# Performance work log

Hardware: AMD Instinct MI355X
Metric: run time of the kernel (lower is better)

## Reference

```python
import jax, jax.numpy as jnp
import numpy as np

B, T, HID = 2, 2048, 2048
H, HKV, HD = 16, 4, 128
GROUPS = H // HKV  # num_query_groups
THETA = 10000.0
SCALE = HD ** -0.5


def setup_inputs() -> dict:
    key = jax.random.key(0)
    ks = jax.random.split(key, 5)
    std = 0.02
    return {
        "x": jax.random.normal(ks[0], (B, T, HID), jnp.float32),
        "Wq": jax.random.normal(ks[1], (HID, H * HD), jnp.float32) * std,
        "Wk": jax.random.normal(ks[2], (HID, HKV * HD), jnp.float32) * std,
        "Wv": jax.random.normal(ks[3], (HID, HKV * HD), jnp.float32) * std,
        "Wo": jax.random.normal(ks[4], (H * HD, HID), jnp.float32) * std,
    }


def _rope(x):
    # x: [B, heads, T, HD]; standard LLaMA-style rotate-half RoPE
    t = x.shape[2]
    inv_freq = 1.0 / (THETA ** (jnp.arange(0, HD, 2, dtype=jnp.float32) / HD))  # [HD/2]
    ang = jnp.arange(t, dtype=jnp.float32)[:, None] * inv_freq[None, :]  # [T, HD/2]
    cos = jnp.concatenate([jnp.cos(ang), jnp.cos(ang)], axis=-1)[None, None]  # [1,1,T,HD]
    sin = jnp.concatenate([jnp.sin(ang), jnp.sin(ang)], axis=-1)[None, None]
    x1, x2 = jnp.split(x, 2, axis=-1)
    rot = jnp.concatenate([-x2, x1], axis=-1)
    return x * cos + rot * sin


def reference(x, Wq, Wk, Wv, Wo):
    b, t, _ = x.shape
    q = (x @ Wq).reshape(b, t, H, HD).transpose(0, 2, 1, 3)      # [B,H,T,HD]
    k = (x @ Wk).reshape(b, t, HKV, HD).transpose(0, 2, 1, 3)    # [B,HKV,T,HD]
    v = (x @ Wv).reshape(b, t, HKV, HD).transpose(0, 2, 1, 3)
    q = _rope(q)
    k = _rope(k)
    # GQA: repeat_interleave kv heads along head dim
    k = jnp.repeat(k, GROUPS, axis=1)  # [B,H,T,HD]
    v = jnp.repeat(v, GROUPS, axis=1)
    scores = jnp.einsum("bhqd,bhkd->bhqk", q, k) * SCALE  # [B,H,T,T]
    causal = jnp.tril(jnp.ones((t, t), dtype=bool))
    scores = jnp.where(causal[None, None], scores, jnp.finfo(scores.dtype).min)
    attn = jax.nn.softmax(scores, axis=-1)
    out = jnp.einsum("bhqk,bhkd->bhqd", attn, v)  # [B,H,T,HD]
    out = out.transpose(0, 2, 1, 3).reshape(b, t, H * HD)
    return out @ Wo
```

## Files before the change

kernel.cpp:

```cpp
#include <hip/hip_runtime.h>
#include <hip/hip_bf16.h>

#define B_   2
#define T_   2048
#define HID_ 2048
#define H_   16
#define HKV_ 4
#define HD_  128
#define NQKV 3072
#define M_   4096
#define SCALE_ 0.08838834764831845f

using f32x4 = __attribute__((ext_vector_type(4))) float;
using s16x8 = __attribute__((ext_vector_type(8))) short;

typedef const __attribute__((address_space(1))) unsigned int* gptr_t;
typedef __attribute__((address_space(3))) unsigned int* lptr_t;

__device__ __forceinline__ unsigned short f2bf(float f) {
  __hip_bfloat16 h = __float2bfloat16(f);
  return *reinterpret_cast<unsigned short*>(&h);
}
__device__ __forceinline__ float bf2f(unsigned short u) {
  union { unsigned int u; float f; } x;
  x.u = ((unsigned int)u) << 16;
  return x.f;
}

__global__ void cast_bf16_k(const float* __restrict__ in, unsigned short* __restrict__ out, int n4) {
  int i = blockIdx.x * 256 + threadIdx.x;
  if (i >= n4) return;
  float4 v = ((const float4*)in)[i];
  ushort4 o;
  o.x = f2bf(v.x); o.y = f2bf(v.y); o.z = f2bf(v.z); o.w = f2bf(v.w);
  ((ushort4*)out)[i] = o;
}

__global__ void transpose_cast_k(const float* __restrict__ in, unsigned short* __restrict__ out,
                                 int R, int C) {
  __shared__ float tile[32][33];
  const int tc = blockIdx.x * 32, tr = blockIdx.y * 32;
  const int lx = threadIdx.x & 31, ly = threadIdx.x >> 5;
#pragma unroll
  for (int i = 0; i < 32; i += 8) tile[ly + i][lx] = in[(long)(tr + ly + i) * C + tc + lx];
  __syncthreads();
#pragma unroll
  for (int i = 0; i < 32; i += 8)
    out[(long)(tc + ly + i) * R + tr + lx] = f2bf(tile[lx][ly + i]);
}

__global__ void transpose_v_k(const unsigned short* __restrict__ qkv, unsigned short* __restrict__ vtp) {
  __shared__ unsigned short tile[32][33];
  const int b = blockIdx.z;
  const int t0 = blockIdx.x * 32, n0 = blockIdx.y * 32;
  const int lx = threadIdx.x & 31, ly = threadIdx.x >> 5;
#pragma unroll
  for (int i = 0; i < 32; i += 8)
    tile[ly + i][lx] = qkv[(long)(b * T_ + t0 + ly + i) * NQKV + 2560 + n0 + lx];
  __syncthreads();
#pragma unroll
  for (int i = 0; i < 32; i += 8)
    vtp[(long)(b * 512 + n0 + ly + i) * T_ + t0 + lx] = tile[lx][ly + i];
}

__global__ void rope_table_k(float* __restrict__ cosT, float* __restrict__ sinT) {
  int idx = blockIdx.x * 256 + threadIdx.x;
  int tt = idx >> 6, i = idx & 63;
  float inv = powf(10000.0f, -(float)i * (1.0f / 64.0f));
  float ang = (float)tt * inv;
  cosT[idx] = cosf(ang);
  sinT[idx] = sinf(ang);
}

__global__ void rope_apply_k(unsigned short* __restrict__ qkv,
                             const float* __restrict__ cosT, const float* __restrict__ sinT) {
  int idx = blockIdx.x * 256 + threadIdx.x;
  int i = idx & 63;
  int r = idx >> 6;
  int hh = r % 20;
  int m = r / 20;
  int tt = m & (T_ - 1);
  int col = (hh < 16) ? hh * 128 + i : 2048 + (hh - 16) * 128 + i;
  float scl = (hh < 16) ? SCALE_ : 1.0f;
  unsigned short* p = qkv + (long)m * NQKV + col;
  float x0 = bf2f(p[0]), x1 = bf2f(p[64]);
  float c = cosT[tt * 64 + i], s = sinT[tt * 64 + i];
  p[0]  = f2bf((x0 * c - x1 * s) * scl);
  p[64] = f2bf((x1 * c + x0 * s) * scl);
}

template <bool BF16OUT>
__global__ __launch_bounds__(256) void gemm_bt(const short* __restrict__ A, const short* __restrict__ Bt,
                                               void* __restrict__ Cv, int M, int N, int K) {
  __shared__ short lA[4096];
  __shared__ short lB[4096];
  const int t = threadIdx.x;
  const int l = t & 63;
  const int w = t >> 6;
  const int wr = (w >> 1) * 64, wc = (w & 1) * 64;
  const int lr = l & 15, lk = (l >> 4) * 8;

  const short* Ag = A + (long)(blockIdx.x * 128 + (t >> 2)) * K + (t & 3) * 8;
  const short* Bg = Bt + (long)(blockIdx.y * 128 + (t >> 2)) * K + (t & 3) * 8;

  f32x4 acc[4][4] = {};

  for (int k0 = 0; k0 < K; k0 += 32) {
    __builtin_amdgcn_global_load_lds((gptr_t)(Ag + k0),                (lptr_t)&lA[t * 8],        16, 0, 0);
    __builtin_amdgcn_global_load_lds((gptr_t)(Ag + (long)64 * K + k0), (lptr_t)&lA[2048 + t * 8], 16, 0, 0);
    __builtin_amdgcn_global_load_lds((gptr_t)(Bg + k0),                (lptr_t)&lB[t * 8],        16, 0, 0);
    __builtin_amdgcn_global_load_lds((gptr_t)(Bg + (long)64 * K + k0), (lptr_t)&lB[2048 + t * 8], 16, 0, 0);
    __syncthreads();
    s16x8 af[4], bfr[4];
#pragma unroll
    for (int m = 0; m < 4; ++m) af[m] = *(const s16x8*)&lA[(wr + m * 16 + lr) * 32 + lk];
#pragma unroll
    for (int n = 0; n < 4; ++n) bfr[n] = *(const s16x8*)&lB[(wc + n * 16 + lr) * 32 + lk];
#pragma unroll
    for (int m = 0; m < 4; ++m)
#pragma unroll
      for (int n = 0; n < 4; ++n)
        acc[m][n] = __builtin_amdgcn_mfma_f32_16x16x32_bf16(af[m], bfr[n], acc[m][n], 0, 0, 0);
    __syncthreads();
  }

#pragma unroll
  for (int m = 0; m < 4; ++m) {
    const int row0 = blockIdx.x * 128 + wr + m * 16 + (l >> 4) * 4;
#pragma unroll
    for (int n = 0; n < 4; ++n) {
      const int col = blockIdx.y * 128 + wc + n * 16 + lr;
#pragma unroll
      for (int r = 0; r < 4; ++r) {
        float v = acc[m][n][r];
        if constexpr (BF16OUT)
          ((unsigned short*)Cv)[(long)(row0 + r) * N + col] = f2bf(v);
        else
          ((float*)Cv)[(long)(row0 + r) * N + col] = v;
      }
    }
  }
}

__global__ __launch_bounds__(256) void attn_kernel(const short* __restrict__ qkv,
                                                   const short* __restrict__ vt,
                                                   unsigned short* __restrict__ outp) {
  const int pj = blockIdx.x;
  const int bh = blockIdx.y;
  const int b = bh >> 4, h = bh & 15, hkv = h >> 2;
  const int tid = threadIdx.x, w = tid >> 6, l = tid & 63;
  const int lr = l & 15, lg = l >> 4;

  __shared__ short lK[2][8192];
  __shared__ short lP[4][16 * 72];

  const short* kb = qkv + (long)(b * T_) * NQKV + 2048 + hkv * HD_;
  const short* vb = vt + (long)(b * 512 + hkv * HD_) * T_;
  short* pw = &lP[w][0];

  auto STAGE = [&](int buf, int kvt) {
#pragma unroll
    for (int i = 0; i < 4; ++i) {
      int flat16 = i * 256 + tid;
      int r = flat16 >> 4;
      int cb = (flat16 & 15) << 4;
      int scb = cb ^ ((r & 7) << 4);
      const short* src = kb + (long)(kvt * 64 + r) * NQKV + (scb >> 1);
      __builtin_amdgcn_global_load_lds((gptr_t)src, (lptr_t)&lK[buf][flat16 * 8], 16, 0, 0);
    }
  };

#pragma unroll 1
  for (int ph = 0; ph < 2; ++ph) {
    const int qtile = ph ? 31 - pj : pj;
    const int ntiles = qtile + 1;

    const short* qp = qkv + (long)(b * T_ + qtile * 64 + w * 16 + lr) * NQKV + h * HD_;
    s16x8 qf[4];
#pragma unroll
    for (int ks = 0; ks < 4; ++ks) qf[ks] = *(const s16x8*)(qp + ks * 32 + lg * 8);

    f32x4 o[8] = {};
    float mrun[4], lrun[4];
#pragma unroll
    for (int r = 0; r < 4; ++r) { mrun[r] = -1e30f; lrun[r] = 0.f; }

    STAGE(0, 0);
    __syncthreads();
    int cur = 0;

    for (int kvt = 0; kvt < ntiles; ++kvt) {
      if (kvt + 1 < ntiles) STAGE(cur ^ 1, kvt + 1);

      const char* lkb = (const char*)&lK[cur][0];
      f32x4 s[4] = {};
#pragma unroll
      for (int nb = 0; nb < 4; ++nb) {
        const int row = nb * 16 + lr;
        const int rb = row * 256;
        const int xr = (row & 7) << 4;
#pragma unroll
        for (int ks = 0; ks < 4; ++ks) {
          s16x8 kf = *(const s16x8*)(lkb + (rb + ((ks * 64 + lg * 16) ^ xr)));
          s[nb] = __builtin_amdgcn_mfma_f32_16x16x32_bf16(qf[ks], kf, s[nb], 0, 0, 0);
        }
      }
      if (kvt == qtile) {
#pragma unroll
        for (int nb = 0; nb < 4; ++nb)
#pragma unroll
          for (int r = 0; r < 4; ++r)
            if (nb * 16 + lr > w * 16 + lg * 4 + r) s[nb][r] = -1e30f;
      }
      float sc[4];
#pragma unroll
      for (int r = 0; r < 4; ++r) {
        float v = fmaxf(fmaxf(s[0][r], s[1][r]), fmaxf(s[2][r], s[3][r]));
        v = fmaxf(v, __shfl_xor(v, 1));
        v = fmaxf(v, __shfl_xor(v, 2));
        v = fmaxf(v, __shfl_xor(v, 4));
        v = fmaxf(v, __shfl_xor(v, 8));
        float mnew = fmaxf(mrun[r], v);
        sc[r] = __expf(mrun[r] - mnew);
        mrun[r] = mnew;
      }
      float ps[4] = {0.f, 0.f, 0.f, 0.f};
#pragma unroll
      for (int nb = 0; nb < 4; ++nb)
#pragma unroll
        for (int r = 0; r < 4; ++r) {
          float p = __expf(s[nb][r] - mrun[r]);
          s[nb][r] = p;
          ps[r] += p;
        }
#pragma unroll
      for (int r = 0; r < 4; ++r) {
        ps[r] += __shfl_xor(ps[r], 1);
        ps[r] += __shfl_xor(ps[r], 2);
        ps[r] += __shfl_xor(ps[r], 4);
        ps[r] += __shfl_xor(ps[r], 8);
        lrun[r] = lrun[r] * sc[r] + ps[r];
      }
#pragma unroll
      for (int db = 0; db < 8; ++db)
#pragma unroll
        for (int r = 0; r < 4; ++r) o[db][r] *= sc[r];
#pragma unroll
      for (int nb = 0; nb < 4; ++nb)
#pragma unroll
        for (int r = 0; r < 4; ++r)
          pw[(lg * 4 + r) * 72 + nb * 16 + lr] = (short)f2bf(s[nb][r]);
#pragma unroll
      for (int ks2 = 0; ks2 < 2; ++ks2) {
        s16x8 pf = *(const s16x8*)&pw[lr * 72 + ks2 * 32 + lg * 8];
#pragma unroll
        for (int db = 0; db < 8; ++db) {
          s16x8 vf = *(const s16x8*)(vb + (long)(db * 16 + lr) * T_ + kvt * 64 + ks2 * 32 + lg * 8);
          o[db] = __builtin_amdgcn_mfma_f32_16x16x32_bf16(pf, vf, o[db], 0, 0, 0);
        }
      }
      __syncthreads();
      cur ^= 1;
    }

    unsigned short* ob = outp + (long)(b * T_ + qtile * 64 + w * 16) * HID_ + h * HD_;
#pragma unroll
    for (int db = 0; db < 8; ++db)
#pragma unroll
      for (int r = 0; r < 4; ++r)
        ob[(long)(lg * 4 + r) * HID_ + db * 16 + lr] = f2bf(o[db][r] / lrun[r]);
  }
}

extern "C" void kernel_launch(void* const* d_in, const int* in_sizes, int n_in,
                              void* d_out, int out_size, void* d_ws, size_t ws_size,
                              hipStream_t stream) {
  (void)in_sizes; (void)n_in; (void)out_size; (void)ws_size;
  const float* x  = (const float*)d_in[0];
  const float* Wq = (const float*)d_in[1];
  const float* Wk = (const float*)d_in[2];
  const float* Wv = (const float*)d_in[3];
  const float* Wo = (const float*)d_in[4];
  float* outp = (float*)d_out;

  char* wsp = (char*)d_ws;
  auto take = [&](size_t bytes) { char* p = wsp; wsp += (bytes + 255) & ~(size_t)255; return p; };
  unsigned short* xb    = (unsigned short*)take((size_t)M_ * HID_ * 2);
  unsigned short* WqkvT = (unsigned short*)take((size_t)NQKV * HID_ * 2);
  unsigned short* WoT   = (unsigned short*)take((size_t)HID_ * HID_ * 2);
  unsigned short* QKV   = (unsigned short*)take((size_t)M_ * NQKV * 2);
  unsigned short* Vtb   = (unsigned short*)take((size_t)1024 * T_ * 2);
  unsigned short* AO    = (unsigned short*)take((size_t)M_ * HID_ * 2);
  float* cosT = (float*)take((size_t)T_ * 64 * 4);
  float* sinT = (float*)take((size_t)T_ * 64 * 4);

  cast_bf16_k<<<8192, 256, 0, stream>>>(x, xb, M_ * HID_ / 4);
  transpose_cast_k<<<dim3(64, 64), 256, 0, stream>>>(Wq, WqkvT, 2048, 2048);
  transpose_cast_k<<<dim3(16, 64), 256, 0, stream>>>(Wk, WqkvT + (size_t)2048 * 2048, 2048, 512);
  transpose_cast_k<<<dim3(16, 64), 256, 0, stream>>>(Wv, WqkvT + (size_t)2560 * 2048, 2048, 512);
  transpose_cast_k<<<dim3(64, 64), 256, 0, stream>>>(Wo, WoT, 2048, 2048);
  rope_table_k<<<512, 256, 0, stream>>>(cosT, sinT);

  gemm_bt<true><<<dim3(32, 24), 256, 0, stream>>>((const short*)xb, (const short*)WqkvT,
                                                  (void*)QKV, M_, NQKV, HID_);
  rope_apply_k<<<(M_ * 20 * 64) / 256, 256, 0, stream>>>(QKV, cosT, sinT);
  transpose_v_k<<<dim3(64, 16, 2), 256, 0, stream>>>(QKV, Vtb);

  attn_kernel<<<dim3(16, 32), 256, 0, stream>>>((const short*)QKV, (const short*)Vtb, AO);

  gemm_bt<false><<<dim3(32, 16), 256, 0, stream>>>((const short*)AO, (const short*)WoT,
                                                   (void*)outp, M_, HID_, HID_);
}
```

Measured before the change: 409.7 us.

## Vectorize cast and RoPE kernels, prefetch V fragments early in attention

The cast kernel now handles 8 floats per thread with 16-byte stores, and the RoPE kernel processes 8 elements per thread using vector loads of bf16 data and cos/sin tables. This cuts the instruction count and gives wider memory transactions. In attention, the V fragments for the whole tile are loaded from global memory at the start of each KV iteration, so their latency overlaps the QK^T MFMAs and softmax instead of sitting inside the PV loop. A launch-bounds occupancy hint of 2 is added. The 16 extra vector registers of V data could raise register pressure or cause spills.

```diff
diff --git a/kernel.cpp b/kernel.cpp
--- a/kernel.cpp
+++ b/kernel.cpp
@@ -13,6 +13,7 @@
 
 using f32x4 = __attribute__((ext_vector_type(4))) float;
 using s16x8 = __attribute__((ext_vector_type(8))) short;
+using u16x8 = __attribute__((ext_vector_type(8))) unsigned short;
 
 typedef const __attribute__((address_space(1))) unsigned int* gptr_t;
 typedef __attribute__((address_space(3))) unsigned int* lptr_t;
@@ -27,13 +28,15 @@
   return x.f;
 }
 
-__global__ void cast_bf16_k(const float* __restrict__ in, unsigned short* __restrict__ out, int n4) {
+__global__ void cast_bf16_k(const float* __restrict__ in, unsigned short* __restrict__ out, int n8) {
   int i = blockIdx.x * 256 + threadIdx.x;
-  if (i >= n4) return;
-  float4 v = ((const float4*)in)[i];
-  ushort4 o;
-  o.x = f2bf(v.x); o.y = f2bf(v.y); o.z = f2bf(v.z); o.w = f2bf(v.w);
-  ((ushort4*)out)[i] = o;
+  if (i >= n8) return;
+  float4 v0 = ((const float4*)in)[i * 2];
+  float4 v1 = ((const float4*)in)[i * 2 + 1];
+  u16x8 o;
+  o[0] = f2bf(v0.x); o[1] = f2bf(v0.y); o[2] = f2bf(v0.z); o[3] = f2bf(v0.w);
+  o[4] = f2bf(v1.x); o[5] = f2bf(v1.y); o[6] = f2bf(v1.z); o[7] = f2bf(v1.w);
+  ((u16x8*)out)[i] = o;
 }
 
 __global__ void transpose_cast_k(const float* __restrict__ in, unsigned short* __restrict__ out,
@@ -75,18 +78,30 @@
 __global__ void rope_apply_k(unsigned short* __restrict__ qkv,
                              const float* __restrict__ cosT, const float* __restrict__ sinT) {
   int idx = blockIdx.x * 256 + threadIdx.x;
-  int i = idx & 63;
-  int r = idx >> 6;
+  int g = idx & 7;
+  int r = idx >> 3;
   int hh = r % 20;
   int m = r / 20;
   int tt = m & (T_ - 1);
-  int col = (hh < 16) ? hh * 128 + i : 2048 + (hh - 16) * 128 + i;
+  int col = ((hh < 16) ? hh * 128 : 2048 + (hh - 16) * 128) + g * 8;
   float scl = (hh < 16) ? SCALE_ : 1.0f;
   unsigned short* p = qkv + (long)m * NQKV + col;
-  float x0 = bf2f(p[0]), x1 = bf2f(p[64]);
-  float c = cosT[tt * 64 + i], s = sinT[tt * 64 + i];
-  p[0]  = f2bf((x0 * c - x1 * s) * scl);
-  p[64] = f2bf((x1 * c + x0 * s) * scl);
+  u16x8 lo = *(const u16x8*)(p);
+  u16x8 hi = *(const u16x8*)(p + 64);
+  const float4* cp = (const float4*)(cosT + tt * 64 + g * 8);
+  const float4* sp = (const float4*)(sinT + tt * 64 + g * 8);
+  float c[8], s[8];
+  { float4 a = cp[0], b = cp[1]; c[0]=a.x;c[1]=a.y;c[2]=a.z;c[3]=a.w;c[4]=b.x;c[5]=b.y;c[6]=b.z;c[7]=b.w; }
+  { float4 a = sp[0], b = sp[1]; s[0]=a.x;s[1]=a.y;s[2]=a.z;s[3]=a.w;s[4]=b.x;s[5]=b.y;s[6]=b.z;s[7]=b.w; }
+  u16x8 olo, ohi;
+#pragma unroll
+  for (int j = 0; j < 8; ++j) {
+    float x0 = bf2f(lo[j]), x1 = bf2f(hi[j]);
+    olo[j] = f2bf((x0 * c[j] - x1 * s[j]) * scl);
+    ohi[j] = f2bf((x1 * c[j] + x0 * s[j]) * scl);
+  }
+  *(u16x8*)(p) = olo;
+  *(u16x8*)(p + 64) = ohi;
 }
 
 template <bool BF16OUT>
@@ -142,9 +157,9 @@
   }
 }
 
-__global__ __launch_bounds__(256) void attn_kernel(const short* __restrict__ qkv,
-                                                   const short* __restrict__ vt,
-                                                   unsigned short* __restrict__ outp) {
+__global__ __launch_bounds__(256, 2) void attn_kernel(const short* __restrict__ qkv,
+                                                      const short* __restrict__ vt,
+                                                      unsigned short* __restrict__ outp) {
   const int pj = blockIdx.x;
   const int bh = blockIdx.y;
   const int b = bh >> 4, h = bh & 15, hkv = h >> 2;
@@ -192,6 +207,13 @@
     for (int kvt = 0; kvt < ntiles; ++kvt) {
       if (kvt + 1 < ntiles) STAGE(cur ^ 1, kvt + 1);
 
+      s16x8 vf[2][8];
+#pragma unroll
+      for (int ks2 = 0; ks2 < 2; ++ks2)
+#pragma unroll
+        for (int db = 0; db < 8; ++db)
+          vf[ks2][db] = *(const s16x8*)(vb + (long)(db * 16 + lr) * T_ + kvt * 64 + ks2 * 32 + lg * 8);
+
       const char* lkb = (const char*)&lK[cur][0];
       f32x4 s[4] = {};
 #pragma unroll
@@ -254,10 +276,8 @@
       for (int ks2 = 0; ks2 < 2; ++ks2) {
         s16x8 pf = *(const s16x8*)&pw[lr * 72 + ks2 * 32 + lg * 8];
 #pragma unroll
-        for (int db = 0; db < 8; ++db) {
-          s16x8 vf = *(const s16x8*)(vb + (long)(db * 16 + lr) * T_ + kvt * 64 + ks2 * 32 + lg * 8);
-          o[db] = __builtin_amdgcn_mfma_f32_16x16x32_bf16(pf, vf, o[db], 0, 0, 0);
-        }
+        for (int db = 0; db < 8; ++db)
+          o[db] = __builtin_amdgcn_mfma_f32_16x16x32_bf16(pf, vf[ks2][db], o[db], 0, 0, 0);
       }
       __syncthreads();
       cur ^= 1;
@@ -294,7 +314,7 @@
   float* cosT = (float*)take((size_t)T_ * 64 * 4);
   float* sinT = (float*)take((size_t)T_ * 64 * 4);
 
-  cast_bf16_k<<<8192, 256, 0, stream>>>(x, xb, M_ * HID_ / 4);
+  cast_bf16_k<<<4096, 256, 0, stream>>>(x, xb, M_ * HID_ / 8);
   transpose_cast_k<<<dim3(64, 64), 256, 0, stream>>>(Wq, WqkvT, 2048, 2048);
   transpose_cast_k<<<dim3(16, 64), 256, 0, stream>>>(Wk, WqkvT + (size_t)2048 * 2048, 2048, 512);
   transpose_cast_k<<<dim3(16, 64), 256, 0, stream>>>(Wv, WqkvT + (size_t)2560 * 2048, 2048, 512);
@@ -303,7 +323,7 @@
 
   gemm_bt<true><<<dim3(32, 24), 256, 0, stream>>>((const short*)xb, (const short*)WqkvT,
                                                   (void*)QKV, M_, NQKV, HID_);
-  rope_apply_k<<<(M_ * 20 * 64) / 256, 256, 0, stream>>>(QKV, cosT, sinT);
+  rope_apply_k<<<(M_ * 20 * 8) / 256, 256, 0, stream>>>(QKV, cosT, sinT);
   transpose_v_k<<<dim3(64, 16, 2), 256, 0, stream>>>(QKV, Vtb);
 
   attn_kernel<<<dim3(16, 32), 256, 0, stream>>>((const short*)QKV, (const short*)Vtb, AO);
```

Result: faster. 398.7 us (-2.7%).
